# Optimization experiments

Hardware: AMD Instinct MI355X
Metric: run time of the kernel (lower is better)

## Reference

```python
import jax, jax.numpy as jnp
import numpy as np


def setup_inputs() -> dict:
    key = jax.random.key(0)
    k1, k2 = jax.random.split(key)
    inputs = jax.random.normal(k1, (32768, 512), dtype=jnp.float32)
    codebook = jax.random.normal(k2, (8192, 512), dtype=jnp.float32)
    return {"inputs": inputs, "codebook": codebook}


def reference(inputs, codebook):
    # inputs: [N, D] (flattened), codebook: [K, D]
    D = codebook.shape[1]
    x = inputs.reshape(-1, D)                          # [N, D]
    cb_sqr = jnp.sum(codebook ** 2, axis=1)            # [K]
    x_sqr = jnp.sum(x ** 2, axis=1, keepdims=True)     # [N, 1]
    distances = (cb_sqr[None, :] + x_sqr) - 2.0 * jnp.einsum('nd,kd->nk', x, codebook)
    soft_distances = jax.nn.softmax(-distances, axis=1)  # [N, K]
    return soft_distances
```

## Files before the change

### kernel.cpp

```cpp
#include <hip/hip_runtime.h>


typedef __attribute__((ext_vector_type(8))) __bf16 bf16x8;
typedef __attribute__((ext_vector_type(4))) float f32x4;

typedef __attribute__((address_space(1))) const void global_cvoid;
typedef __attribute__((address_space(3))) void lds_void;

__device__ inline unsigned short f32_to_bf16_rne(float f) {
    unsigned int u = __float_as_uint(f);
    unsigned int r = u + 0x7FFFu + ((u >> 16) & 1u);
    return (unsigned short)(r >> 16);
}
__device__ inline float bf16u_to_f32(unsigned short h) {
    return __uint_as_float(((unsigned int)h) << 16);
}

__global__ void split_kernel(const float* __restrict__ in,
                             unsigned short* __restrict__ hi,
                             unsigned short* __restrict__ lo, int n4) {
    int i = blockIdx.x * blockDim.x + threadIdx.x;
    int stride = gridDim.x * blockDim.x;
    for (; i < n4; i += stride) {
        float4 v = reinterpret_cast<const float4*>(in)[i];
        float vv[4] = {v.x, v.y, v.z, v.w};
        ushort4 hv, lv;
        unsigned short h[4], l[4];
#pragma unroll
        for (int j = 0; j < 4; ++j) {
            h[j] = f32_to_bf16_rne(vv[j]);
            float r = vv[j] - bf16u_to_f32(h[j]);
            l[j] = f32_to_bf16_rne(r);
        }
        hv.x = h[0]; hv.y = h[1]; hv.z = h[2]; hv.w = h[3];
        lv.x = l[0]; lv.y = l[1]; lv.z = l[2]; lv.w = l[3];
        reinterpret_cast<ushort4*>(hi)[i] = hv;
        reinterpret_cast<ushort4*>(lo)[i] = lv;
    }
}

__global__ void rowsq_kernel(const float* __restrict__ cb, float* __restrict__ out) {
    int row = blockIdx.x * 4 + (threadIdx.x >> 6);
    int lane = threadIdx.x & 63;
    const float4* p = reinterpret_cast<const float4*>(cb + (size_t)row * 512);
    float4 a = p[lane];
    float4 b = p[lane + 64];
    float s = a.x * a.x + a.y * a.y + a.z * a.z + a.w * a.w +
              b.x * b.x + b.y * b.y + b.z * b.z + b.w * b.w;
#pragma unroll
    for (int o = 32; o >= 1; o >>= 1) s += __shfl_xor(s, o);
    if (lane == 0) out[row] = s;
}


#define RD_A(bq_)                                                                 \
    { _Pragma("unroll") for (int m = 0; m < 4; ++m)                               \
        afr[m] = *(const bf16x8*)&ldsA[bq_][(a_slot + m * 64) * 8]; }

#define RD_B(bq_)                                                                 \
    { _Pragma("unroll") for (int n = 0; n < 4; ++n)                               \
        bfr[n] = *(const bf16x8*)&ldsB[bq_][(b_slot + n * 64) * 8]; }

#define ST(tt_)                                                                   \
    { int prod_ = (tt_) >> 4, ko_ = ((tt_) & 15) * 32, bq_ = (tt_) & 1;           \
      const unsigned short* Asrc_ = (prod_ < 2 ? Ah : Al) + arow0 + ko_;          \
      const unsigned short* Bsrc_ = (prod_ == 1 ? Bl : Bh) + brow0 + ko_;         \
      __builtin_amdgcn_global_load_lds((global_cvoid*)(Asrc_ + goffA),            \
          (lds_void*)&ldsA[bq_][slA], 16, 0, 0);                                  \
      _Pragma("unroll") for (int j = 0; j < 2; ++j)                               \
          __builtin_amdgcn_global_load_lds((global_cvoid*)(Bsrc_ + goffB[j]),     \
              (lds_void*)&ldsB[bq_][slB[j]], 16, 0, 0);                           \
    }

#define MM_ALL()                                                                  \
    { _Pragma("unroll") for (int m = 0; m < 4; ++m)                               \
      _Pragma("unroll") for (int n = 0; n < 4; ++n)                               \
          acc[m][n] = __builtin_amdgcn_mfma_f32_16x16x32_bf16(                    \
              afr[m], bfr[n], acc[m][n], 0, 0, 0); }

template <int F16>
__global__ __launch_bounds__(512, 4) void gemm_kernel(
    const unsigned short* __restrict__ Ah, const unsigned short* __restrict__ Al,
    const unsigned short* __restrict__ Bh, const unsigned short* __restrict__ Bl,
    const float* __restrict__ cbq, float* __restrict__ outf,
    unsigned short* __restrict__ p16, float* __restrict__ max_part,
    float* __restrict__ sum_part) {
    __shared__ __align__(16) unsigned short ldsA[2][4096];
    __shared__ __align__(16) unsigned short ldsB[2][8192];

    const int t = threadIdx.x;
    const int lane = t & 63;
    const int w = t >> 6;
    const int wm = w >> 2, wn = w & 3;
    const int fr = lane & 15, fg = lane >> 4;

    int bid = blockIdx.x;
    int swz = (bid & 7) * 1024 + (bid >> 3);
    const int bm = swz >> 5, bn = swz & 31;
    const int row0 = bm * 128, col0 = bn * 256;
    const size_t arow0 = (size_t)row0 * 512;
    const size_t brow0 = (size_t)col0 * 512;

    const int xsl = fg ^ ((fr >> 1) & 3);
    const int a_slot = (wm * 64 + fr) * 4 + xsl;
    const int b_slot = (wn * 64 + fr) * 4 + xsl;

    int goffA, slA, goffB[2], slB[2];
    {
        int s = t, r_ = s >> 2, cp_ = s & 3;
        goffA = r_ * 512 + (cp_ ^ ((r_ >> 1) & 3)) * 8;
        slA = s * 8;
    }
#pragma unroll
    for (int j = 0; j < 2; ++j) {
        int s = j * 512 + t, r_ = s >> 2, cp_ = s & 3;
        goffB[j] = r_ * 512 + (cp_ ^ ((r_ >> 1) & 3)) * 8;
        slB[j] = s * 8;
    }

    f32x4 acc[4][4] = {};
    bf16x8 afr[4], bfr[4];

    ST(0);
    asm volatile("s_waitcnt vmcnt(0)\n\ts_barrier" ::: "memory");

    for (int tt = 0; tt < 48; ++tt) {
        const int bq = tt & 1;
        RD_B(bq);
        RD_A(bq);
        if (tt < 47) ST(tt + 1);
        MM_ALL();
        asm volatile("s_waitcnt vmcnt(0)\n\ts_barrier" ::: "memory");
    }

    float* redm = (float*)&ldsA[0][0];
    float* reds = redm + 512;

    float cq[4];
#pragma unroll
    for (int n = 0; n < 4; ++n) cq[n] = cbq[col0 + wn * 64 + n * 16 + fr];
#pragma unroll
    for (int m = 0; m < 4; ++m)
#pragma unroll
        for (int n = 0; n < 4; ++n)
#pragma unroll
            for (int r = 0; r < 4; ++r)
                acc[m][n][r] = 2.0f * acc[m][n][r] - cq[n];

    float rmx[4][4];
#pragma unroll
    for (int m = 0; m < 4; ++m)
#pragma unroll
        for (int r = 0; r < 4; ++r) {
            float v = fmaxf(fmaxf(acc[m][0][r], acc[m][1][r]),
                            fmaxf(acc[m][2][r], acc[m][3][r]));
#pragma unroll
            for (int o = 1; o < 16; o <<= 1) v = fmaxf(v, __shfl_xor(v, o));
            rmx[m][r] = v;
        }
    __syncthreads();
    if (fr == 0) {
#pragma unroll
        for (int m = 0; m < 4; ++m)
#pragma unroll
            for (int r = 0; r < 4; ++r)
                redm[wn * 128 + wm * 64 + m * 16 + fg * 4 + r] = rmx[m][r];
    }
    __syncthreads();
#pragma unroll
    for (int m = 0; m < 4; ++m)
#pragma unroll
        for (int r = 0; r < 4; ++r) {
            int row = wm * 64 + m * 16 + fg * 4 + r;
            rmx[m][r] = fmaxf(fmaxf(redm[row], redm[128 + row]),
                              fmaxf(redm[256 + row], redm[384 + row]));
        }
#pragma unroll
    for (int m = 0; m < 4; ++m)
#pragma unroll
        for (int r = 0; r < 4; ++r) {
            float s = 0.f;
#pragma unroll
            for (int n = 0; n < 4; ++n) s += __expf(acc[m][n][r] - rmx[m][r]);
#pragma unroll
            for (int o = 1; o < 16; o <<= 1) s += __shfl_xor(s, o);
            if (fr == 0) reds[wn * 128 + wm * 64 + m * 16 + fg * 4 + r] = s;
        }
    __syncthreads();
    if (wn == 0 && fr == 0) {
#pragma unroll
        for (int m = 0; m < 4; ++m)
#pragma unroll
            for (int r = 0; r < 4; ++r) {
                int row = wm * 64 + m * 16 + fg * 4 + r;
                size_t gr = (size_t)(row0 + row);
                max_part[gr * 32 + bn] = rmx[m][r];
                sum_part[gr * 32 + bn] =
                    reds[row] + reds[128 + row] + reds[256 + row] + reds[384 + row];
            }
    }
#pragma unroll
    for (int m = 0; m < 4; ++m)
#pragma unroll
        for (int n = 0; n < 4; ++n)
#pragma unroll
            for (int r = 0; r < 4; ++r) {
                size_t gr = (size_t)(row0 + wm * 64 + m * 16 + fg * 4 + r);
                size_t gi = gr * 8192 + col0 + wn * 64 + n * 16 + fr;
                if constexpr (F16) {
                    union { _Float16 h; unsigned short u; } cv;
                    cv.h = (_Float16)__expf(acc[m][n][r] - rmx[m][r]);
                    p16[gi] = cv.u;
                } else {
                    outf[gi] = acc[m][n][r];
                }
            }
}

__global__ void combine_kernel(const float* __restrict__ max_part,
                               const float* __restrict__ sum_part,
                               float* __restrict__ row_m, float* __restrict__ row_is,
                               float* __restrict__ scale, int do_scale) {
    int row = blockIdx.x * 8 + (threadIdx.x >> 5);
    int l = threadIdx.x & 31;
    size_t off = (size_t)row * 32 + l;
    float m = max_part[off];
    float s = sum_part[off];
    float gm = m;
#pragma unroll
    for (int o = 16; o >= 1; o >>= 1) gm = fmaxf(gm, __shfl_xor(gm, o, 32));
    float c = s * __expf(m - gm);
#pragma unroll
    for (int o = 16; o >= 1; o >>= 1) c += __shfl_xor(c, o, 32);
    float inv = 1.0f / c;
    if (do_scale) scale[off] = __expf(m - gm) * inv;
    if (l == 0) {
        row_m[row] = gm;
        row_is[row] = inv;
    }
}

__global__ void norm_kernel(float* __restrict__ out, const float* __restrict__ row_m,
                            const float* __restrict__ row_is) {
    size_t i = (size_t)blockIdx.x * blockDim.x + threadIdx.x;
    size_t stride = (size_t)gridDim.x * blockDim.x;
    const size_t n4 = 268435456ull / 4;
    float4* p = reinterpret_cast<float4*>(out);
    for (; i < n4; i += stride) {
        int row = (int)(i >> 11);
        float m = row_m[row];
        float is = row_is[row];
        float4 v = p[i];
        v.x = __expf(v.x - m) * is;
        v.y = __expf(v.y - m) * is;
        v.z = __expf(v.z - m) * is;
        v.w = __expf(v.w - m) * is;
        p[i] = v;
    }
}

__global__ void norm_f16_kernel(const unsigned short* __restrict__ p16,
                                const float* __restrict__ scale,
                                float* __restrict__ out) {
    size_t i = (size_t)blockIdx.x * blockDim.x + threadIdx.x;
    size_t stride = (size_t)gridDim.x * blockDim.x;
    const size_t ng = 268435456ull / 8;
    const uint4* src = reinterpret_cast<const uint4*>(p16);
    float4* dst = reinterpret_cast<float4*>(out);
    for (; i < ng; i += stride) {
        int row = (int)(i >> 10);
        int bn = (int)((i >> 5) & 31);
        float s = scale[(size_t)row * 32 + bn];
        union { uint4 u; _Float16 h[8]; } cv;
        cv.u = src[i];
        float4 o1, o2;
        o1.x = (float)cv.h[0] * s; o1.y = (float)cv.h[1] * s;
        o1.z = (float)cv.h[2] * s; o1.w = (float)cv.h[3] * s;
        o2.x = (float)cv.h[4] * s; o2.y = (float)cv.h[5] * s;
        o2.z = (float)cv.h[6] * s; o2.w = (float)cv.h[7] * s;
        dst[i * 2] = o1;
        dst[i * 2 + 1] = o2;
    }
}

extern "C" void kernel_launch(void* const* d_in, const int* in_sizes, int n_in,
                              void* d_out, int out_size, void* d_ws, size_t ws_size,
                              hipStream_t stream) {
    const float* x = (const float*)d_in[0];
    const float* cb = (const float*)d_in[1];
    float* out = (float*)d_out;
    char* ws = (char*)d_ws;

    unsigned short* Xh = (unsigned short*)(ws);
    unsigned short* Xl = (unsigned short*)(ws + 33554432ull);
    unsigned short* Ch = (unsigned short*)(ws + 67108864ull);
    unsigned short* Cl = (unsigned short*)(ws + 75497472ull);
    float* cbq       = (float*)(ws + 83886080ull);
    float* max_part  = (float*)(ws + 83918848ull);
    float* sum_part  = (float*)(ws + 88113152ull);
    float* row_m     = (float*)(ws + 92307456ull);
    float* row_is    = (float*)(ws + 92438528ull);
    float* scale     = (float*)(ws + 92569600ull);
    unsigned short* p16 = (unsigned short*)(ws + 96763904ull);

    const bool f16path = (ws_size >= 633634816ull);

    split_kernel<<<2048, 256, 0, stream>>>(x, Xh, Xl, 32768 * 512 / 4);
    split_kernel<<<1024, 256, 0, stream>>>(cb, Ch, Cl, 8192 * 512 / 4);
    rowsq_kernel<<<2048, 256, 0, stream>>>(cb, cbq);
    if (f16path) {
        gemm_kernel<1><<<8192, 512, 0, stream>>>(Xh, Xl, Ch, Cl, cbq, out, p16,
                                                 max_part, sum_part);
        combine_kernel<<<4096, 256, 0, stream>>>(max_part, sum_part, row_m, row_is,
                                                 scale, 1);
        norm_f16_kernel<<<4096, 256, 0, stream>>>(p16, scale, out);
    } else {
        gemm_kernel<0><<<8192, 512, 0, stream>>>(Xh, Xl, Ch, Cl, cbq, out, p16,
                                                 max_part, sum_part);
        combine_kernel<<<4096, 256, 0, stream>>>(max_part, sum_part, row_m, row_is,
                                                 scale, 0);
        norm_kernel<<<4096, 256, 0, stream>>>(out, row_m, row_is);
    }
}
```

Before: 1.468 ms.

## Triple-buffer GEMM LDS staging and use nontemporal stores for softmax streams

Moves the GEMM main loop from double to triple buffering in LDS. Global-to-LDS loads are now issued two tiles ahead, and the wait is relaxed to vmcnt(3) so one tile's loads stay in flight across the barrier. The fp16 intermediate writes and the normalize kernel's loads and stores become nontemporal to limit cache pollution on the large streamed buffers. The extra LDS buffer raises shared memory per block from 48KB to 72KB, which may lower occupancy under launch_bounds(512,4).

```diff
diff --git a/kernel.cpp b/kernel.cpp
--- a/kernel.cpp
+++ b/kernel.cpp
@@ -3,6 +3,7 @@
 
 typedef __attribute__((ext_vector_type(8))) __bf16 bf16x8;
 typedef __attribute__((ext_vector_type(4))) float f32x4;
+typedef __attribute__((ext_vector_type(4))) unsigned int u32x4;
 
 typedef __attribute__((address_space(1))) const void global_cvoid;
 typedef __attribute__((address_space(3))) void lds_void;
@@ -61,8 +62,8 @@
     { _Pragma("unroll") for (int n = 0; n < 4; ++n)                               \
         bfr[n] = *(const bf16x8*)&ldsB[bq_][(b_slot + n * 64) * 8]; }
 
-#define ST(tt_)                                                                   \
-    { int prod_ = (tt_) >> 4, ko_ = ((tt_) & 15) * 32, bq_ = (tt_) & 1;           \
+#define ST(tt_, bq_)                                                              \
+    { int prod_ = (tt_) >> 4, ko_ = ((tt_) & 15) * 32;                            \
       const unsigned short* Asrc_ = (prod_ < 2 ? Ah : Al) + arow0 + ko_;          \
       const unsigned short* Bsrc_ = (prod_ == 1 ? Bl : Bh) + brow0 + ko_;         \
       __builtin_amdgcn_global_load_lds((global_cvoid*)(Asrc_ + goffA),            \
@@ -85,8 +86,8 @@
     const float* __restrict__ cbq, float* __restrict__ outf,
     unsigned short* __restrict__ p16, float* __restrict__ max_part,
     float* __restrict__ sum_part) {
-    __shared__ __align__(16) unsigned short ldsA[2][4096];
-    __shared__ __align__(16) unsigned short ldsB[2][8192];
+    __shared__ __align__(16) unsigned short ldsA[3][4096];
+    __shared__ __align__(16) unsigned short ldsB[3][8192];
 
     const int t = threadIdx.x;
     const int lane = t & 63;
@@ -121,16 +122,25 @@
     f32x4 acc[4][4] = {};
     bf16x8 afr[4], bfr[4];
 
-    ST(0);
-    asm volatile("s_waitcnt vmcnt(0)\n\ts_barrier" ::: "memory");
-
+    ST(0, 0);
+    ST(1, 1);
+    asm volatile("s_waitcnt vmcnt(3)\n\ts_barrier" ::: "memory");
+
+    int bq = 0, sq = 2;
     for (int tt = 0; tt < 48; ++tt) {
-        const int bq = tt & 1;
         RD_B(bq);
         RD_A(bq);
-        if (tt < 47) ST(tt + 1);
+        if (tt < 46) ST(tt + 2, sq);
         MM_ALL();
-        asm volatile("s_waitcnt vmcnt(0)\n\ts_barrier" ::: "memory");
+        if (tt < 46) {
+            asm volatile("s_waitcnt vmcnt(3) lgkmcnt(0)\n\ts_barrier" ::: "memory");
+        } else if (tt == 46) {
+            asm volatile("s_waitcnt vmcnt(0) lgkmcnt(0)\n\ts_barrier" ::: "memory");
+        } else {
+            asm volatile("s_waitcnt lgkmcnt(0)\n\ts_barrier" ::: "memory");
+        }
+        bq = (bq == 2) ? 0 : bq + 1;
+        sq = (sq == 2) ? 0 : sq + 1;
     }
 
     float* redm = (float*)&ldsA[0][0];
@@ -210,7 +220,7 @@
                 if constexpr (F16) {
                     union { _Float16 h; unsigned short u; } cv;
                     cv.h = (_Float16)__expf(acc[m][n][r] - rmx[m][r]);
-                    p16[gi] = cv.u;
+                    __builtin_nontemporal_store(cv.u, &p16[gi]);
                 } else {
                     outf[gi] = acc[m][n][r];
                 }
@@ -265,21 +275,21 @@
     size_t i = (size_t)blockIdx.x * blockDim.x + threadIdx.x;
     size_t stride = (size_t)gridDim.x * blockDim.x;
     const size_t ng = 268435456ull / 8;
-    const uint4* src = reinterpret_cast<const uint4*>(p16);
-    float4* dst = reinterpret_cast<float4*>(out);
+    const u32x4* src = reinterpret_cast<const u32x4*>(p16);
+    f32x4* dst = reinterpret_cast<f32x4*>(out);
     for (; i < ng; i += stride) {
         int row = (int)(i >> 10);
         int bn = (int)((i >> 5) & 31);
         float s = scale[(size_t)row * 32 + bn];
-        union { uint4 u; _Float16 h[8]; } cv;
-        cv.u = src[i];
-        float4 o1, o2;
+        union { u32x4 u; _Float16 h[8]; } cv;
+        cv.u = __builtin_nontemporal_load(&src[i]);
+        f32x4 o1, o2;
         o1.x = (float)cv.h[0] * s; o1.y = (float)cv.h[1] * s;
         o1.z = (float)cv.h[2] * s; o1.w = (float)cv.h[3] * s;
         o2.x = (float)cv.h[4] * s; o2.y = (float)cv.h[5] * s;
         o2.z = (float)cv.h[6] * s; o2.w = (float)cv.h[7] * s;
-        dst[i * 2] = o1;
-        dst[i * 2 + 1] = o2;
+        __builtin_nontemporal_store(o1, &dst[i * 2]);
+        __builtin_nontemporal_store(o2, &dst[i * 2 + 1]);
     }
 }
 
```

After: 1.498 ms. 1.02x slower.

## Replace split-bf16 GEMM with two-level int8 per-row quantized MFMA GEMM

Applied to the files above, without the earlier changes.

Each row of the inputs and of the codebook is quantized to a 16-bit fixed-point value with its own per-row scale, then split into hi and lo int8 bytes. The distance GEMM now runs as three int8 MFMA products (hi*hi, hi*lo, lo*hi), folded into fp32 with factors of 256, instead of three bf16 products. This halves the bytes per element and uses the faster int8 MFMA rate. The main loop also moves to a triple-buffered LDS pipeline that keeps one load stage in flight, and occupancy drops to 2 blocks per CU. The risk is accuracy: the per-row quantization error may not match the reference closely enough once the softmax amplifies it.

```diff
diff --git a/kernel.cpp b/kernel.cpp
--- a/kernel.cpp
+++ b/kernel.cpp
@@ -1,70 +1,70 @@
 #include <hip/hip_runtime.h>
 
 
-typedef __attribute__((ext_vector_type(8))) __bf16 bf16x8;
+typedef __attribute__((ext_vector_type(4))) int i32x4;
 typedef __attribute__((ext_vector_type(4))) float f32x4;
 
 typedef __attribute__((address_space(1))) const void global_cvoid;
 typedef __attribute__((address_space(3))) void lds_void;
 
-__device__ inline unsigned short f32_to_bf16_rne(float f) {
-    unsigned int u = __float_as_uint(f);
-    unsigned int r = u + 0x7FFFu + ((u >> 16) & 1u);
-    return (unsigned short)(r >> 16);
-}
-__device__ inline float bf16u_to_f32(unsigned short h) {
-    return __uint_as_float(((unsigned int)h) << 16);
-}
-
-__global__ void split_kernel(const float* __restrict__ in,
-                             unsigned short* __restrict__ hi,
-                             unsigned short* __restrict__ lo, int n4) {
-    int i = blockIdx.x * blockDim.x + threadIdx.x;
-    int stride = gridDim.x * blockDim.x;
-    for (; i < n4; i += stride) {
-        float4 v = reinterpret_cast<const float4*>(in)[i];
-        float vv[4] = {v.x, v.y, v.z, v.w};
-        ushort4 hv, lv;
-        unsigned short h[4], l[4];
-#pragma unroll
-        for (int j = 0; j < 4; ++j) {
-            h[j] = f32_to_bf16_rne(vv[j]);
-            float r = vv[j] - bf16u_to_f32(h[j]);
-            l[j] = f32_to_bf16_rne(r);
-        }
-        hv.x = h[0]; hv.y = h[1]; hv.z = h[2]; hv.w = h[3];
-        lv.x = l[0]; lv.y = l[1]; lv.z = l[2]; lv.w = l[3];
-        reinterpret_cast<ushort4*>(hi)[i] = hv;
-        reinterpret_cast<ushort4*>(lo)[i] = lv;
-    }
-}
-
-__global__ void rowsq_kernel(const float* __restrict__ cb, float* __restrict__ out) {
+template <int CB>
+__global__ void quant_kernel(const float* __restrict__ in, char* __restrict__ hi,
+                             char* __restrict__ lo, float* __restrict__ finv,
+                             float* __restrict__ sqout) {
     int row = blockIdx.x * 4 + (threadIdx.x >> 6);
     int lane = threadIdx.x & 63;
-    const float4* p = reinterpret_cast<const float4*>(cb + (size_t)row * 512);
+    const float4* p = reinterpret_cast<const float4*>(in + (size_t)row * 512);
     float4 a = p[lane];
     float4 b = p[lane + 64];
-    float s = a.x * a.x + a.y * a.y + a.z * a.z + a.w * a.w +
-              b.x * b.x + b.y * b.y + b.z * b.z + b.w * b.w;
-#pragma unroll
-    for (int o = 32; o >= 1; o >>= 1) s += __shfl_xor(s, o);
-    if (lane == 0) out[row] = s;
+    float va[8] = {a.x, a.y, a.z, a.w, b.x, b.y, b.z, b.w};
+    float mx = 1e-20f, sq = 0.f;
+#pragma unroll
+    for (int j = 0; j < 8; ++j) {
+        mx = fmaxf(mx, fabsf(va[j]));
+        sq += va[j] * va[j];
+    }
+#pragma unroll
+    for (int o = 32; o >= 1; o >>= 1) {
+        mx = fmaxf(mx, __shfl_xor(mx, o));
+        sq += __shfl_xor(sq, o);
+    }
+    float F = 32639.0f / mx;
+    int qh[8], ql[8];
+#pragma unroll
+    for (int j = 0; j < 8; ++j) {
+        float qf = fminf(fmaxf(va[j] * F, -32639.f), 32639.f);
+        int q = (int)rintf(qf);
+        int h = (q + 128) >> 8;
+        qh[j] = h;
+        ql[j] = q - (h << 8);
+    }
+    unsigned ph0 = (qh[0] & 255) | ((qh[1] & 255) << 8) | ((qh[2] & 255) << 16) | ((qh[3] & 255) << 24);
+    unsigned ph1 = (qh[4] & 255) | ((qh[5] & 255) << 8) | ((qh[6] & 255) << 16) | ((qh[7] & 255) << 24);
+    unsigned pl0 = (ql[0] & 255) | ((ql[1] & 255) << 8) | ((ql[2] & 255) << 16) | ((ql[3] & 255) << 24);
+    unsigned pl1 = (ql[4] & 255) | ((ql[5] & 255) << 8) | ((ql[6] & 255) << 16) | ((ql[7] & 255) << 24);
+    *(unsigned*)(hi + (size_t)row * 512 + lane * 4) = ph0;
+    *(unsigned*)(hi + (size_t)row * 512 + (lane + 64) * 4) = ph1;
+    *(unsigned*)(lo + (size_t)row * 512 + lane * 4) = pl0;
+    *(unsigned*)(lo + (size_t)row * 512 + (lane + 64) * 4) = pl1;
+    if (lane == 0) {
+        finv[row] = mx * (1.0f / 32639.0f);
+        if (CB) sqout[row] = sq;
+    }
 }
 
 
 #define RD_A(bq_)                                                                 \
     { _Pragma("unroll") for (int m = 0; m < 4; ++m)                               \
-        afr[m] = *(const bf16x8*)&ldsA[bq_][(a_slot + m * 64) * 8]; }
+        afr[m] = *(const i32x4*)&ldsA[bq_][(a_slot + m * 64) * 16]; }
 
 #define RD_B(bq_)                                                                 \
     { _Pragma("unroll") for (int n = 0; n < 4; ++n)                               \
-        bfr[n] = *(const bf16x8*)&ldsB[bq_][(b_slot + n * 64) * 8]; }
-
-#define ST(tt_)                                                                   \
-    { int prod_ = (tt_) >> 4, ko_ = ((tt_) & 15) * 32, bq_ = (tt_) & 1;           \
-      const unsigned short* Asrc_ = (prod_ < 2 ? Ah : Al) + arow0 + ko_;          \
-      const unsigned short* Bsrc_ = (prod_ == 1 ? Bl : Bh) + brow0 + ko_;         \
+        bfr[n] = *(const i32x4*)&ldsB[bq_][(b_slot + n * 64) * 16]; }
+
+#define ST(tt_, bq_)                                                              \
+    { int prod_ = (tt_) >> 3, ko_ = ((tt_) & 7) * 64;                             \
+      const char* Asrc_ = (prod_ < 2 ? Xh : Xl) + arow0 + ko_;                    \
+      const char* Bsrc_ = ((prod_ & 1) ? Cl : Ch) + brow0 + ko_;                  \
       __builtin_amdgcn_global_load_lds((global_cvoid*)(Asrc_ + goffA),            \
           (lds_void*)&ldsA[bq_][slA], 16, 0, 0);                                  \
       _Pragma("unroll") for (int j = 0; j < 2; ++j)                               \
@@ -75,18 +75,27 @@
 #define MM_ALL()                                                                  \
     { _Pragma("unroll") for (int m = 0; m < 4; ++m)                               \
       _Pragma("unroll") for (int n = 0; n < 4; ++n)                               \
-          acc[m][n] = __builtin_amdgcn_mfma_f32_16x16x32_bf16(                    \
-              afr[m], bfr[n], acc[m][n], 0, 0, 0); }
+          accP[m][n] = __builtin_amdgcn_mfma_i32_16x16x64_i8(                     \
+              afr[m], bfr[n], accP[m][n], 0, 0, 0); }
+
+#define FOLD()                                                                    \
+    { _Pragma("unroll") for (int m = 0; m < 4; ++m)                               \
+      _Pragma("unroll") for (int n = 0; n < 4; ++n) {                             \
+        _Pragma("unroll") for (int r = 0; r < 4; ++r)                             \
+            fACC[m][n][r] = fACC[m][n][r] * 256.0f + (float)accP[m][n][r];        \
+        accP[m][n] = (i32x4){0, 0, 0, 0};                                         \
+      } }
 
 template <int F16>
-__global__ __launch_bounds__(512, 4) void gemm_kernel(
-    const unsigned short* __restrict__ Ah, const unsigned short* __restrict__ Al,
-    const unsigned short* __restrict__ Bh, const unsigned short* __restrict__ Bl,
-    const float* __restrict__ cbq, float* __restrict__ outf,
+__global__ __launch_bounds__(512, 2) void gemm_kernel(
+    const char* __restrict__ Xh, const char* __restrict__ Xl,
+    const char* __restrict__ Ch, const char* __restrict__ Cl,
+    const float* __restrict__ cbq, const float* __restrict__ fxinv,
+    const float* __restrict__ fcinv, float* __restrict__ outf,
     unsigned short* __restrict__ p16, float* __restrict__ max_part,
     float* __restrict__ sum_part) {
-    __shared__ __align__(16) unsigned short ldsA[2][4096];
-    __shared__ __align__(16) unsigned short ldsB[2][8192];
+    __shared__ __align__(16) char ldsA[3][8192];
+    __shared__ __align__(16) char ldsB[3][16384];
 
     const int t = threadIdx.x;
     const int lane = t & 63;
@@ -108,52 +117,75 @@
     int goffA, slA, goffB[2], slB[2];
     {
         int s = t, r_ = s >> 2, cp_ = s & 3;
-        goffA = r_ * 512 + (cp_ ^ ((r_ >> 1) & 3)) * 8;
-        slA = s * 8;
+        goffA = r_ * 512 + (cp_ ^ ((r_ >> 1) & 3)) * 16;
+        slA = s * 16;
     }
 #pragma unroll
     for (int j = 0; j < 2; ++j) {
         int s = j * 512 + t, r_ = s >> 2, cp_ = s & 3;
-        goffB[j] = r_ * 512 + (cp_ ^ ((r_ >> 1) & 3)) * 8;
-        slB[j] = s * 8;
-    }
-
-    f32x4 acc[4][4] = {};
-    bf16x8 afr[4], bfr[4];
-
-    ST(0);
-    asm volatile("s_waitcnt vmcnt(0)\n\ts_barrier" ::: "memory");
-
-    for (int tt = 0; tt < 48; ++tt) {
-        const int bq = tt & 1;
+        goffB[j] = r_ * 512 + (cp_ ^ ((r_ >> 1) & 3)) * 16;
+        slB[j] = s * 16;
+    }
+
+    i32x4 accP[4][4] = {};
+    f32x4 fACC[4][4] = {};
+    i32x4 afr[4], bfr[4];
+
+    ST(0, 0);
+    ST(1, 1);
+    asm volatile("s_waitcnt vmcnt(3)\n\ts_barrier" ::: "memory");
+
+    int bq = 0, sq = 2;
+    for (int tt = 0; tt < 32; ++tt) {
         RD_B(bq);
         RD_A(bq);
-        if (tt < 47) ST(tt + 1);
+        if (tt < 30) ST(tt + 2, sq);
         MM_ALL();
-        asm volatile("s_waitcnt vmcnt(0)\n\ts_barrier" ::: "memory");
-    }
+        if (tt == 7 || tt == 23) FOLD();
+        if (tt < 30) {
+            asm volatile("s_waitcnt vmcnt(3) lgkmcnt(0)\n\ts_barrier" ::: "memory");
+        } else if (tt == 30) {
+            asm volatile("s_waitcnt vmcnt(0) lgkmcnt(0)\n\ts_barrier" ::: "memory");
+        } else {
+            asm volatile("s_waitcnt lgkmcnt(0)\n\ts_barrier" ::: "memory");
+        }
+        bq = (bq == 2) ? 0 : bq + 1;
+        sq = (sq == 2) ? 0 : sq + 1;
+    }
+    FOLD();
 
     float* redm = (float*)&ldsA[0][0];
     float* reds = redm + 512;
 
-    float cq[4];
-#pragma unroll
-    for (int n = 0; n < 4; ++n) cq[n] = cbq[col0 + wn * 64 + n * 16 + fr];
+    float cq[4], fcv[4];
+#pragma unroll
+    for (int n = 0; n < 4; ++n) {
+        int col = col0 + wn * 64 + n * 16 + fr;
+        cq[n] = cbq[col];
+        fcv[n] = fcinv[col];
+    }
+    float fxv[4][4];
+#pragma unroll
+    for (int m = 0; m < 4; ++m)
+#pragma unroll
+        for (int r = 0; r < 4; ++r)
+            fxv[m][r] = fxinv[row0 + wm * 64 + m * 16 + fg * 4 + r];
+
 #pragma unroll
     for (int m = 0; m < 4; ++m)
 #pragma unroll
         for (int n = 0; n < 4; ++n)
 #pragma unroll
             for (int r = 0; r < 4; ++r)
-                acc[m][n][r] = 2.0f * acc[m][n][r] - cq[n];
+                fACC[m][n][r] = 2.0f * fxv[m][r] * fcv[n] * fACC[m][n][r] - cq[n];
 
     float rmx[4][4];
 #pragma unroll
     for (int m = 0; m < 4; ++m)
 #pragma unroll
         for (int r = 0; r < 4; ++r) {
-            float v = fmaxf(fmaxf(acc[m][0][r], acc[m][1][r]),
-                            fmaxf(acc[m][2][r], acc[m][3][r]));
+            float v = fmaxf(fmaxf(fACC[m][0][r], fACC[m][1][r]),
+                            fmaxf(fACC[m][2][r], fACC[m][3][r]));
 #pragma unroll
             for (int o = 1; o < 16; o <<= 1) v = fmaxf(v, __shfl_xor(v, o));
             rmx[m][r] = v;
@@ -181,7 +213,7 @@
         for (int r = 0; r < 4; ++r) {
             float s = 0.f;
 #pragma unroll
-            for (int n = 0; n < 4; ++n) s += __expf(acc[m][n][r] - rmx[m][r]);
+            for (int n = 0; n < 4; ++n) s += __expf(fACC[m][n][r] - rmx[m][r]);
 #pragma unroll
             for (int o = 1; o < 16; o <<= 1) s += __shfl_xor(s, o);
             if (fr == 0) reds[wn * 128 + wm * 64 + m * 16 + fg * 4 + r] = s;
@@ -209,10 +241,10 @@
                 size_t gi = gr * 8192 + col0 + wn * 64 + n * 16 + fr;
                 if constexpr (F16) {
                     union { _Float16 h; unsigned short u; } cv;
-                    cv.h = (_Float16)__expf(acc[m][n][r] - rmx[m][r]);
+                    cv.h = (_Float16)__expf(fACC[m][n][r] - rmx[m][r]);
                     p16[gi] = cv.u;
                 } else {
-                    outf[gi] = acc[m][n][r];
+                    outf[gi] = fACC[m][n][r];
                 }
             }
 }
@@ -291,32 +323,33 @@
     float* out = (float*)d_out;
     char* ws = (char*)d_ws;
 
-    unsigned short* Xh = (unsigned short*)(ws);
-    unsigned short* Xl = (unsigned short*)(ws + 33554432ull);
-    unsigned short* Ch = (unsigned short*)(ws + 67108864ull);
-    unsigned short* Cl = (unsigned short*)(ws + 75497472ull);
-    float* cbq       = (float*)(ws + 83886080ull);
-    float* max_part  = (float*)(ws + 83918848ull);
-    float* sum_part  = (float*)(ws + 88113152ull);
-    float* row_m     = (float*)(ws + 92307456ull);
-    float* row_is    = (float*)(ws + 92438528ull);
-    float* scale     = (float*)(ws + 92569600ull);
-    unsigned short* p16 = (unsigned short*)(ws + 96763904ull);
-
-    const bool f16path = (ws_size >= 633634816ull);
-
-    split_kernel<<<2048, 256, 0, stream>>>(x, Xh, Xl, 32768 * 512 / 4);
-    split_kernel<<<1024, 256, 0, stream>>>(cb, Ch, Cl, 8192 * 512 / 4);
-    rowsq_kernel<<<2048, 256, 0, stream>>>(cb, cbq);
+    char* Xh        = ws;
+    char* Xl        = ws + 16777216ull;
+    char* Ch        = ws + 33554432ull;
+    char* Cl        = ws + 37748736ull;
+    float* cbq      = (float*)(ws + 41943040ull);
+    float* fxinv    = (float*)(ws + 41975808ull);
+    float* fcinv    = (float*)(ws + 42106880ull);
+    float* max_part = (float*)(ws + 42139648ull);
+    float* sum_part = (float*)(ws + 46333952ull);
+    float* row_m    = (float*)(ws + 50528256ull);
+    float* row_is   = (float*)(ws + 50659328ull);
+    float* scale    = (float*)(ws + 50790400ull);
+    unsigned short* p16 = (unsigned short*)(ws + 54984704ull);
+
+    const bool f16path = (ws_size >= 591855616ull);
+
+    quant_kernel<0><<<8192, 256, 0, stream>>>(x, Xh, Xl, fxinv, nullptr);
+    quant_kernel<1><<<2048, 256, 0, stream>>>(cb, Ch, Cl, fcinv, cbq);
     if (f16path) {
-        gemm_kernel<1><<<8192, 512, 0, stream>>>(Xh, Xl, Ch, Cl, cbq, out, p16,
-                                                 max_part, sum_part);
+        gemm_kernel<1><<<8192, 512, 0, stream>>>(Xh, Xl, Ch, Cl, cbq, fxinv, fcinv,
+                                                 out, p16, max_part, sum_part);
         combine_kernel<<<4096, 256, 0, stream>>>(max_part, sum_part, row_m, row_is,
                                                  scale, 1);
         norm_f16_kernel<<<4096, 256, 0, stream>>>(p16, scale, out);
     } else {
-        gemm_kernel<0><<<8192, 512, 0, stream>>>(Xh, Xl, Ch, Cl, cbq, out, p16,
-                                                 max_part, sum_part);
+        gemm_kernel<0><<<8192, 512, 0, stream>>>(Xh, Xl, Ch, Cl, cbq, fxinv, fcinv,
+                                                 out, p16, max_part, sum_part);
         combine_kernel<<<4096, 256, 0, stream>>>(max_part, sum_part, row_m, row_is,
                                                  scale, 0);
         norm_kernel<<<4096, 256, 0, stream>>>(out, row_m, row_is);
```

After: 1.444 ms. Within noise of the previous version (-1.6%).

## Triple-buffer LDS tiles and split K-step into two phases with prefetch depth two

Applied to the files above, without the earlier changes.

Moves from double to triple LDS buffering so global-to-LDS loads run two k-steps ahead, waiting on vmcnt(3) instead of draining all loads each iteration. Each k-step is split into two halves, each with its own A-fragment reads, partial load issue and a group of MFMAs raised with s_setprio, interleaved with barriers. The aim is to hide global load latency behind MFMA work. In exchange LDS use rises by half, which may limit occupancy at launch_bounds(512,4), and extra barriers add sync overhead.

```diff
diff --git a/kernel.cpp b/kernel.cpp
--- a/kernel.cpp
+++ b/kernel.cpp
@@ -53,30 +53,36 @@
 }
 
 
-#define RD_A(bq_)                                                                 \
-    { _Pragma("unroll") for (int m = 0; m < 4; ++m)                               \
-        afr[m] = *(const bf16x8*)&ldsA[bq_][(a_slot + m * 64) * 8]; }
+#define RD_A(h_, bq_)                                                             \
+    { _Pragma("unroll") for (int j = 0; j < 2; ++j)                               \
+        afr[j] = *(const bf16x8*)&ldsA[bq_][(a_slot + ((h_) * 2 + j) * 64) * 8]; }
 
 #define RD_B(bq_)                                                                 \
     { _Pragma("unroll") for (int n = 0; n < 4; ++n)                               \
         bfr[n] = *(const bf16x8*)&ldsB[bq_][(b_slot + n * 64) * 8]; }
 
-#define ST(tt_)                                                                   \
-    { int prod_ = (tt_) >> 4, ko_ = ((tt_) & 15) * 32, bq_ = (tt_) & 1;           \
+#define ST_P0(tt_, bq_)                                                           \
+    { int prod_ = (tt_) >> 4, ko_ = ((tt_) & 15) * 32;                            \
       const unsigned short* Asrc_ = (prod_ < 2 ? Ah : Al) + arow0 + ko_;          \
       const unsigned short* Bsrc_ = (prod_ == 1 ? Bl : Bh) + brow0 + ko_;         \
       __builtin_amdgcn_global_load_lds((global_cvoid*)(Asrc_ + goffA),            \
           (lds_void*)&ldsA[bq_][slA], 16, 0, 0);                                  \
-      _Pragma("unroll") for (int j = 0; j < 2; ++j)                               \
-          __builtin_amdgcn_global_load_lds((global_cvoid*)(Bsrc_ + goffB[j]),     \
-              (lds_void*)&ldsB[bq_][slB[j]], 16, 0, 0);                           \
-    }
-
-#define MM_ALL()                                                                  \
-    { _Pragma("unroll") for (int m = 0; m < 4; ++m)                               \
+      __builtin_amdgcn_global_load_lds((global_cvoid*)(Bsrc_ + goffB[0]),         \
+          (lds_void*)&ldsB[bq_][slB[0]], 16, 0, 0);                               \
+    }
+
+#define ST_P1(tt_, bq_)                                                           \
+    { int prod_ = (tt_) >> 4, ko_ = ((tt_) & 15) * 32;                            \
+      const unsigned short* Bsrc_ = (prod_ == 1 ? Bl : Bh) + brow0 + ko_;         \
+      __builtin_amdgcn_global_load_lds((global_cvoid*)(Bsrc_ + goffB[1]),         \
+          (lds_void*)&ldsB[bq_][slB[1]], 16, 0, 0);                               \
+    }
+
+#define MM(h_)                                                                    \
+    { _Pragma("unroll") for (int j = 0; j < 2; ++j)                               \
       _Pragma("unroll") for (int n = 0; n < 4; ++n)                               \
-          acc[m][n] = __builtin_amdgcn_mfma_f32_16x16x32_bf16(                    \
-              afr[m], bfr[n], acc[m][n], 0, 0, 0); }
+          acc[(h_) * 2 + j][n] = __builtin_amdgcn_mfma_f32_16x16x32_bf16(         \
+              afr[j], bfr[n], acc[(h_) * 2 + j][n], 0, 0, 0); }
 
 template <int F16>
 __global__ __launch_bounds__(512, 4) void gemm_kernel(
@@ -85,8 +91,8 @@
     const float* __restrict__ cbq, float* __restrict__ outf,
     unsigned short* __restrict__ p16, float* __restrict__ max_part,
     float* __restrict__ sum_part) {
-    __shared__ __align__(16) unsigned short ldsA[2][4096];
-    __shared__ __align__(16) unsigned short ldsB[2][8192];
+    __shared__ __align__(16) unsigned short ldsA[3][4096];
+    __shared__ __align__(16) unsigned short ldsB[3][8192];
 
     const int t = threadIdx.x;
     const int lane = t & 63;
@@ -119,18 +125,35 @@
     }
 
     f32x4 acc[4][4] = {};
-    bf16x8 afr[4], bfr[4];
-
-    ST(0);
-    asm volatile("s_waitcnt vmcnt(0)\n\ts_barrier" ::: "memory");
-
+    bf16x8 afr[2], bfr[4];
+
+    ST_P0(0, 0); ST_P1(0, 0);
+    ST_P0(1, 1); ST_P1(1, 1);
+    asm volatile("s_waitcnt vmcnt(3)\n\ts_barrier" ::: "memory");
+
+    int bq = 0, sq = 2;
     for (int tt = 0; tt < 48; ++tt) {
-        const int bq = tt & 1;
         RD_B(bq);
-        RD_A(bq);
-        if (tt < 47) ST(tt + 1);
-        MM_ALL();
-        asm volatile("s_waitcnt vmcnt(0)\n\ts_barrier" ::: "memory");
+        RD_A(0, bq);
+        if (tt < 46) ST_P0(tt + 2, sq);
+        __builtin_amdgcn_s_barrier();
+        asm volatile("s_waitcnt lgkmcnt(0)" ::: "memory");
+        __builtin_amdgcn_s_setprio(1); MM(0); __builtin_amdgcn_s_setprio(0);
+        __builtin_amdgcn_s_barrier();
+        RD_A(1, bq);
+        if (tt < 46) ST_P1(tt + 2, sq);
+        __builtin_amdgcn_s_barrier();
+        asm volatile("s_waitcnt lgkmcnt(0)" ::: "memory");
+        __builtin_amdgcn_s_setprio(1); MM(1); __builtin_amdgcn_s_setprio(0);
+        if (tt < 46) {
+            asm volatile("s_waitcnt vmcnt(3)\n\ts_barrier" ::: "memory");
+        } else if (tt == 46) {
+            asm volatile("s_waitcnt vmcnt(0)\n\ts_barrier" ::: "memory");
+        } else {
+            __builtin_amdgcn_s_barrier();
+        }
+        bq = (bq == 2) ? 0 : bq + 1;
+        sq = (sq == 2) ? 0 : sq + 1;
     }
 
     float* redm = (float*)&ldsA[0][0];
```

After: 1.499 ms. 1.02x slower.
